# Optimization experiments

Measured on AMD Instinct MI355X. Metric: run time of the kernel, lower is better.

Reference implementation:

```python
import jax, jax.numpy as jnp
import numpy as np

S = 7; B = 2; C = 20; N = 8; BS = 16384
LAMBDA_COORD = 5.0; LAMBDA_NOOBJ = 0.5
EPS = 1e-6


def setup_inputs() -> dict:
    key = jax.random.key(0)
    k1, k2, k3 = jax.random.split(key, 3)
    outputs = jax.random.uniform(k1, (BS, S, S, B * 5 + C), dtype=jnp.float32)
    gt_boxes = jax.random.uniform(k2, (BS, N, 4), dtype=jnp.float32)
    gt_labels = jax.random.randint(k3, (BS, N), 0, C)
    return {"outputs": outputs, "gt_boxes": gt_boxes, "gt_labels": gt_labels}


def _pairwise_iou(pred_xywh, gt_boxes):
    # pred_xywh: [bs,S,S,B,4] (center x,y,w,h); gt_boxes: [bs,N,4] -> iou [bs,S,S,B,N]
    p = pred_xywh[..., None, :]                       # [bs,S,S,B,1,4]
    g = gt_boxes[:, None, None, None, :, :]           # [bs,1,1,1,N,4]
    px1, py1 = p[..., 0] - p[..., 2] / 2, p[..., 1] - p[..., 3] / 2
    px2, py2 = p[..., 0] + p[..., 2] / 2, p[..., 1] + p[..., 3] / 2
    gx1, gy1 = g[..., 0] - g[..., 2] / 2, g[..., 1] - g[..., 3] / 2
    gx2, gy2 = g[..., 0] + g[..., 2] / 2, g[..., 1] + g[..., 3] / 2
    iw = jnp.clip(jnp.minimum(px2, gx2) - jnp.maximum(px1, gx1), 0.0)
    ih = jnp.clip(jnp.minimum(py2, gy2) - jnp.maximum(py1, gy1), 0.0)
    inter = iw * ih
    union = p[..., 2] * p[..., 3] + g[..., 2] * g[..., 3] - inter
    return inter / (union + EPS)


def reference(outputs, gt_boxes, gt_labels):
    bs = outputs.shape[0]
    pred = outputs[..., : B * 5].reshape(bs, S, S, B, 5)   # [bs,S,S,B,5]
    pred_xywh, pred_conf = pred[..., :4], pred[..., 4]
    pred_cls = outputs[..., B * 5:]                        # [bs,S,S,C]

    iou = _pairwise_iou(pred_xywh, gt_boxes)               # [bs,S,S,B,N]

    # Original loop: for each gt j, if iou(:,j).max() > best -> best_iou, best_box_idx = argmax over B.
    iou_max_over_b = jnp.max(iou, axis=3)                  # [bs,S,S,N]
    j_star = jnp.argmax(iou_max_over_b, axis=-1)
    best_iou = jnp.max(iou_max_over_b, axis=-1)            # [bs,S,S]
    iou_at_j = jnp.take_along_axis(iou, j_star[..., None, None], axis=4)[..., 0]  # [bs,S,S,B]
    best_b = jnp.argmax(iou_at_j, axis=-1)                 # [bs,S,S] in [0,B)

    # Faithful to source: gt_boxes indexed by best_box_idx (the pred-box index), requires N >= B.
    gt_sel = jnp.take_along_axis(
        jnp.broadcast_to(gt_boxes[:, None, None], (bs, S, S, N, 4)),
        best_b[..., None, None], axis=3)[..., 0, :]        # [bs,S,S,4]
    pred_sel = jnp.take_along_axis(pred, best_b[..., None, None], axis=3)[..., 0, :]  # [bs,S,S,5]

    loc = ((pred_sel[..., 0] - gt_sel[..., 0]) ** 2
           + (pred_sel[..., 1] - gt_sel[..., 1]) ** 2
           + (jnp.sqrt(pred_sel[..., 2]) - jnp.sqrt(gt_sel[..., 2])) ** 2
           + (jnp.sqrt(pred_sel[..., 3]) - jnp.sqrt(gt_sel[..., 3])) ** 2)
    loc = LAMBDA_COORD * loc                               # [bs,S,S]

    conf_obj = (pred_sel[..., 4] - best_iou) ** 2          # [bs,S,S]

    # Classification: mean cross-entropy of the cell's class logits vs all gt labels
    logp = jax.nn.log_softmax(pred_cls, axis=-1)           # [bs,S,S,C]
    lab = jnp.broadcast_to(gt_labels[:, None, None, :], (bs, S, S, N))
    ce = -jnp.mean(jnp.take_along_axis(logp, lab, axis=3), axis=-1)  # [bs,S,S]

    noobj = LAMBDA_NOOBJ * jnp.sum(pred_conf ** 2, axis=-1)  # [bs,S,S]

    has_obj = best_iou > 0.0
    per_cell = jnp.where(has_obj, loc + conf_obj + ce, noobj)
    return jnp.sum(per_cell) / bs
```

## Files before the change

### kernel.cpp

```cpp
#include <hip/hip_runtime.h>

namespace {

constexpr int kS = 7;
constexpr int kC = 20;
constexpr int kN = 8;
constexpr int kBS = 16384;
constexpr int kCells = kBS * kS * kS;
constexpr int kTile = 256;
constexpr int kBlocks = kCells / kTile;
constexpr int kF = 30;
constexpr float kLambdaCoord = 5.0f;
constexpr float kLambdaNoobj = 0.5f;
constexpr float kEps = 1e-6f;

typedef const __attribute__((address_space(1))) unsigned int gu32;
typedef __attribute__((address_space(3))) unsigned int lu32;

__global__ __launch_bounds__(256) void yolo_loss_kernel(
    const float* __restrict__ outputs,
    const float* __restrict__ gt_boxes,
    const int* __restrict__ gt_labels,
    float* __restrict__ partials) {
  __shared__ float lds[kTile * kF];
  __shared__ float ws[4];

  const int tid = threadIdx.x;
  const int lane = tid & 63;
  const int w = tid >> 6;

  {
    const char* srcb = reinterpret_cast<const char*>(outputs) +
                       ((size_t)blockIdx.x * kTile + (size_t)w * 64) * 120;
    char* dstb = reinterpret_cast<char*>(lds) + w * 7680;
#pragma unroll
    for (int k = 0; k < 7; ++k) {
      __builtin_amdgcn_global_load_lds((gu32*)(srcb + k * 1024 + lane * 16),
                                       (lu32*)(dstb + k * 1024 + lane * 16),
                                       16, 0, 0);
    }
    if (lane < 32) {
      __builtin_amdgcn_global_load_lds((gu32*)(srcb + 7168 + lane * 16),
                                       (lu32*)(dstb + 7168 + lane * 16),
                                       16, 0, 0);
    }
  }

  const int c = blockIdx.x * kTile + tid;
  const int bs = c / (kS * kS);
  float g[kN][4];
  const float4* gb4 =
      reinterpret_cast<const float4*>(gt_boxes + (size_t)bs * kN * 4);
#pragma unroll
  for (int n = 0; n < kN; ++n) {
    float4 v = gb4[n];
    g[n][0] = v.x; g[n][1] = v.y; g[n][2] = v.z; g[n][3] = v.w;
  }
  const int4* lb4 = reinterpret_cast<const int4*>(gt_labels + (size_t)bs * kN);
  const int4 lab0 = lb4[0];
  const int4 lab1 = lb4[1];

  float gx1[kN], gx2[kN], gy1[kN], gy2[kN], ga[kN];
#pragma unroll
  for (int n = 0; n < kN; ++n) {
    gx1[n] = g[n][0] - g[n][2] * 0.5f;
    gx2[n] = g[n][0] + g[n][2] * 0.5f;
    gy1[n] = g[n][1] - g[n][3] * 0.5f;
    gy2[n] = g[n][1] + g[n][3] * 0.5f;
    ga[n]  = g[n][2] * g[n][3];
  }

  asm volatile("s_waitcnt vmcnt(0)" ::: "memory");

  const float* x = lds + tid * kF;

  float iou[2][kN];
#pragma unroll
  for (int b = 0; b < 2; ++b) {
    const float px = x[b * 5 + 0], py = x[b * 5 + 1];
    const float pw = x[b * 5 + 2], ph = x[b * 5 + 3];
    const float px1 = px - pw * 0.5f, px2 = px + pw * 0.5f;
    const float py1 = py - ph * 0.5f, py2 = py + ph * 0.5f;
    const float parea = pw * ph;
#pragma unroll
    for (int n = 0; n < kN; ++n) {
      const float iw = fmaxf(fminf(px2, gx2[n]) - fmaxf(px1, gx1[n]), 0.0f);
      const float ih = fmaxf(fminf(py2, gy2[n]) - fmaxf(py1, gy1[n]), 0.0f);
      const float inter = iw * ih;
      const float uni = parea + ga[n] - inter;
      iou[b][n] = inter * __builtin_amdgcn_rcpf(uni + kEps);
    }
  }

  float best_iou = -1.0f;
  float i0j = 0.0f, i1j = 0.0f;
#pragma unroll
  for (int n = 0; n < kN; ++n) {
    const float m = fmaxf(iou[0][n], iou[1][n]);
    if (m > best_iou) { best_iou = m; i0j = iou[0][n]; i1j = iou[1][n]; }
  }
  const int bb = (i1j > i0j) ? 1 : 0;

  const float gsx = bb ? g[1][0] : g[0][0];
  const float gsy = bb ? g[1][1] : g[0][1];
  const float gsw = bb ? g[1][2] : g[0][2];
  const float gsh = bb ? g[1][3] : g[0][3];
  const float psx = bb ? x[5] : x[0];
  const float psy = bb ? x[6] : x[1];
  const float psw = bb ? x[7] : x[2];
  const float psh = bb ? x[8] : x[3];
  const float psc = bb ? x[9] : x[4];

  const float dx = psx - gsx;
  const float dy = psy - gsy;
  const float dw = __builtin_amdgcn_sqrtf(psw) - __builtin_amdgcn_sqrtf(gsw);
  const float dh = __builtin_amdgcn_sqrtf(psh) - __builtin_amdgcn_sqrtf(gsh);
  const float loc = kLambdaCoord * (dx * dx + dy * dy + dw * dw + dh * dh);
  const float conf_obj = (psc - best_iou) * (psc - best_iou);

  float se = 0.0f;
#pragma unroll
  for (int k = 0; k < kC; ++k) se += __expf(x[10 + k]);
  const float lse = __logf(se);

  float ce = 0.0f;
  ce += x[10 + lab0.x] + x[10 + lab0.y] + x[10 + lab0.z] + x[10 + lab0.w];
  ce += x[10 + lab1.x] + x[10 + lab1.y] + x[10 + lab1.z] + x[10 + lab1.w];
  ce = -(ce - 8.0f * lse) * (1.0f / kN);

  const float noobj = kLambdaNoobj * (x[4] * x[4] + x[9] * x[9]);

  float val = (best_iou > 0.0f) ? (loc + conf_obj + ce) : noobj;

#pragma unroll
  for (int off = 32; off > 0; off >>= 1) val += __shfl_down(val, off, 64);
  if (lane == 0) ws[w] = val;
  __syncthreads();
  if (tid == 0) {
    partials[blockIdx.x] = ws[0] + ws[1] + ws[2] + ws[3];
  }
}

__global__ __launch_bounds__(256) void reduce_kernel(
    const float* __restrict__ partials, float* __restrict__ out) {
  float s = 0.0f;
  for (int i = threadIdx.x; i < kBlocks; i += 256) s += partials[i];
#pragma unroll
  for (int off = 32; off > 0; off >>= 1) s += __shfl_down(s, off, 64);
  __shared__ float ws[4];
  const int lane = threadIdx.x & 63;
  const int wid = threadIdx.x >> 6;
  if (lane == 0) ws[wid] = s;
  __syncthreads();
  if (threadIdx.x == 0) {
    out[0] = (ws[0] + ws[1] + ws[2] + ws[3]) * (1.0f / kBS);
  }
}

}

extern "C" void kernel_launch(void* const* d_in, const int* in_sizes, int n_in,
                              void* d_out, int out_size, void* d_ws, size_t ws_size,
                              hipStream_t stream) {
  const float* outputs = (const float*)d_in[0];
  const float* gt_boxes = (const float*)d_in[1];
  const int* gt_labels = (const int*)d_in[2];
  float* out = (float*)d_out;
  float* partials = (float*)d_ws;

  yolo_loss_kernel<<<kBlocks, kTile, 0, stream>>>(outputs, gt_boxes, gt_labels, partials);
  reduce_kernel<<<1, 256, 0, stream>>>(partials, out);
}
```

Measured before the change: 27.13 us.

## Process two tiles per block with double-buffered LDS and overlapped compute

Each block now stages two 256-cell tiles into separate LDS buffers and uses a partial vmcnt wait. Compute on the first tile can then start while the second tile's async global-to-LDS loads are still in flight. Per-sample gt values, including the sqrt of the first two box widths and heights, are packed once per tile, and the cross-entropy expression is simplified. The grid is halved, and LDS per block doubles to about 60KB, which together with higher register pressure may reduce occupancy and latency hiding.

```diff
diff --git a/kernel.cpp b/kernel.cpp
--- a/kernel.cpp
+++ b/kernel.cpp
@@ -8,7 +8,8 @@
 constexpr int kBS = 16384;
 constexpr int kCells = kBS * kS * kS;
 constexpr int kTile = 256;
-constexpr int kBlocks = kCells / kTile;
+constexpr int kTiles = kCells / kTile;
+constexpr int kBlocks = kTiles / 2;
 constexpr int kF = 30;
 constexpr float kLambdaCoord = 5.0f;
 constexpr float kLambdaNoobj = 0.5f;
@@ -17,63 +18,51 @@
 typedef const __attribute__((address_space(1))) unsigned int gu32;
 typedef __attribute__((address_space(3))) unsigned int lu32;
 
-__global__ __launch_bounds__(256) void yolo_loss_kernel(
-    const float* __restrict__ outputs,
-    const float* __restrict__ gt_boxes,
-    const int* __restrict__ gt_labels,
-    float* __restrict__ partials) {
-  __shared__ float lds[kTile * kF];
-  __shared__ float ws[4];
-
-  const int tid = threadIdx.x;
-  const int lane = tid & 63;
-  const int w = tid >> 6;
-
-  {
-    const char* srcb = reinterpret_cast<const char*>(outputs) +
-                       ((size_t)blockIdx.x * kTile + (size_t)w * 64) * 120;
-    char* dstb = reinterpret_cast<char*>(lds) + w * 7680;
-#pragma unroll
-    for (int k = 0; k < 7; ++k) {
-      __builtin_amdgcn_global_load_lds((gu32*)(srcb + k * 1024 + lane * 16),
-                                       (lu32*)(dstb + k * 1024 + lane * 16),
-                                       16, 0, 0);
-    }
-    if (lane < 32) {
-      __builtin_amdgcn_global_load_lds((gu32*)(srcb + 7168 + lane * 16),
-                                       (lu32*)(dstb + 7168 + lane * 16),
-                                       16, 0, 0);
-    }
-  }
-
-  const int c = blockIdx.x * kTile + tid;
-  const int bs = c / (kS * kS);
-  float g[kN][4];
-  const float4* gb4 =
-      reinterpret_cast<const float4*>(gt_boxes + (size_t)bs * kN * 4);
+__device__ __forceinline__ void stage_wave(const char* __restrict__ srcb,
+                                           char* dstb, int lane) {
+#pragma unroll
+  for (int k = 0; k < 7; ++k) {
+    __builtin_amdgcn_global_load_lds((gu32*)(srcb + k * 1024 + lane * 16),
+                                     (lu32*)(dstb + k * 1024 + lane * 16),
+                                     16, 0, 0);
+  }
+  if (lane < 32) {
+    __builtin_amdgcn_global_load_lds((gu32*)(srcb + 7168 + lane * 16),
+                                     (lu32*)(dstb + 7168 + lane * 16),
+                                     16, 0, 0);
+  }
+}
+
+struct GtPack {
+  float g0x, g0y, g1x, g1y;
+  float sg0w, sg0h, sg1w, sg1h;
+  float gx1[kN], gx2[kN], gy1[kN], gy2[kN], ga[kN];
+  int4 la, lb;
+};
+
+__device__ __forceinline__ GtPack make_pack(const float g[kN][4], int4 la,
+                                            int4 lb) {
+  GtPack P;
+  P.g0x = g[0][0]; P.g0y = g[0][1];
+  P.g1x = g[1][0]; P.g1y = g[1][1];
+  P.sg0w = __builtin_amdgcn_sqrtf(g[0][2]);
+  P.sg0h = __builtin_amdgcn_sqrtf(g[0][3]);
+  P.sg1w = __builtin_amdgcn_sqrtf(g[1][2]);
+  P.sg1h = __builtin_amdgcn_sqrtf(g[1][3]);
 #pragma unroll
   for (int n = 0; n < kN; ++n) {
-    float4 v = gb4[n];
-    g[n][0] = v.x; g[n][1] = v.y; g[n][2] = v.z; g[n][3] = v.w;
-  }
-  const int4* lb4 = reinterpret_cast<const int4*>(gt_labels + (size_t)bs * kN);
-  const int4 lab0 = lb4[0];
-  const int4 lab1 = lb4[1];
-
-  float gx1[kN], gx2[kN], gy1[kN], gy2[kN], ga[kN];
-#pragma unroll
-  for (int n = 0; n < kN; ++n) {
-    gx1[n] = g[n][0] - g[n][2] * 0.5f;
-    gx2[n] = g[n][0] + g[n][2] * 0.5f;
-    gy1[n] = g[n][1] - g[n][3] * 0.5f;
-    gy2[n] = g[n][1] + g[n][3] * 0.5f;
-    ga[n]  = g[n][2] * g[n][3];
-  }
-
-  asm volatile("s_waitcnt vmcnt(0)" ::: "memory");
-
-  const float* x = lds + tid * kF;
-
+    P.gx1[n] = g[n][0] - g[n][2] * 0.5f;
+    P.gx2[n] = g[n][0] + g[n][2] * 0.5f;
+    P.gy1[n] = g[n][1] - g[n][3] * 0.5f;
+    P.gy2[n] = g[n][1] + g[n][3] * 0.5f;
+    P.ga[n]  = g[n][2] * g[n][3];
+  }
+  P.la = la; P.lb = lb;
+  return P;
+}
+
+__device__ __forceinline__ float cell_loss(const float* __restrict__ x,
+                                           const GtPack& P) {
   float iou[2][kN];
 #pragma unroll
   for (int b = 0; b < 2; ++b) {
@@ -84,10 +73,10 @@
     const float parea = pw * ph;
 #pragma unroll
     for (int n = 0; n < kN; ++n) {
-      const float iw = fmaxf(fminf(px2, gx2[n]) - fmaxf(px1, gx1[n]), 0.0f);
-      const float ih = fmaxf(fminf(py2, gy2[n]) - fmaxf(py1, gy1[n]), 0.0f);
+      const float iw = fmaxf(fminf(px2, P.gx2[n]) - fmaxf(px1, P.gx1[n]), 0.0f);
+      const float ih = fmaxf(fminf(py2, P.gy2[n]) - fmaxf(py1, P.gy1[n]), 0.0f);
       const float inter = iw * ih;
-      const float uni = parea + ga[n] - inter;
+      const float uni = parea + P.ga[n] - inter;
       iou[b][n] = inter * __builtin_amdgcn_rcpf(uni + kEps);
     }
   }
@@ -101,10 +90,10 @@
   }
   const int bb = (i1j > i0j) ? 1 : 0;
 
-  const float gsx = bb ? g[1][0] : g[0][0];
-  const float gsy = bb ? g[1][1] : g[0][1];
-  const float gsw = bb ? g[1][2] : g[0][2];
-  const float gsh = bb ? g[1][3] : g[0][3];
+  const float gsx = bb ? P.g1x : P.g0x;
+  const float gsy = bb ? P.g1y : P.g0y;
+  const float sgw = bb ? P.sg1w : P.sg0w;
+  const float sgh = bb ? P.sg1h : P.sg0h;
   const float psx = bb ? x[5] : x[0];
   const float psy = bb ? x[6] : x[1];
   const float psw = bb ? x[7] : x[2];
@@ -113,8 +102,8 @@
 
   const float dx = psx - gsx;
   const float dy = psy - gsy;
-  const float dw = __builtin_amdgcn_sqrtf(psw) - __builtin_amdgcn_sqrtf(gsw);
-  const float dh = __builtin_amdgcn_sqrtf(psh) - __builtin_amdgcn_sqrtf(gsh);
+  const float dw = __builtin_amdgcn_sqrtf(psw) - sgw;
+  const float dh = __builtin_amdgcn_sqrtf(psh) - sgh;
   const float loc = kLambdaCoord * (dx * dx + dy * dy + dw * dw + dh * dh);
   const float conf_obj = (psc - best_iou) * (psc - best_iou);
 
@@ -123,14 +112,73 @@
   for (int k = 0; k < kC; ++k) se += __expf(x[10 + k]);
   const float lse = __logf(se);
 
-  float ce = 0.0f;
-  ce += x[10 + lab0.x] + x[10 + lab0.y] + x[10 + lab0.z] + x[10 + lab0.w];
-  ce += x[10 + lab1.x] + x[10 + lab1.y] + x[10 + lab1.z] + x[10 + lab1.w];
-  ce = -(ce - 8.0f * lse) * (1.0f / kN);
+  float s8 = 0.0f;
+  s8 += x[10 + P.la.x] + x[10 + P.la.y] + x[10 + P.la.z] + x[10 + P.la.w];
+  s8 += x[10 + P.lb.x] + x[10 + P.lb.y] + x[10 + P.lb.z] + x[10 + P.lb.w];
+  const float ce = lse - 0.125f * s8;
 
   const float noobj = kLambdaNoobj * (x[4] * x[4] + x[9] * x[9]);
 
-  float val = (best_iou > 0.0f) ? (loc + conf_obj + ce) : noobj;
+  return (best_iou > 0.0f) ? (loc + conf_obj + ce) : noobj;
+}
+
+__global__ __launch_bounds__(256) void yolo_loss_kernel(
+    const float* __restrict__ outputs,
+    const float* __restrict__ gt_boxes,
+    const int* __restrict__ gt_labels,
+    float* __restrict__ partials) {
+  __shared__ float lds[2][kTile * kF];
+  __shared__ float ws[4];
+
+  const int tid = threadIdx.x;
+  const int lane = tid & 63;
+  const int w = tid >> 6;
+
+  const int t0 = blockIdx.x * 2;
+  const int c0 = t0 * kTile + tid;
+  const int c1 = c0 + kTile;
+  const int bs0 = c0 / (kS * kS);
+  const int bs1 = c1 / (kS * kS);
+
+  float g0[kN][4], g1[kN][4];
+  {
+    const float4* a = reinterpret_cast<const float4*>(gt_boxes + (size_t)bs0 * kN * 4);
+    const float4* b = reinterpret_cast<const float4*>(gt_boxes + (size_t)bs1 * kN * 4);
+#pragma unroll
+    for (int n = 0; n < kN; ++n) {
+      float4 v = a[n];
+      g0[n][0] = v.x; g0[n][1] = v.y; g0[n][2] = v.z; g0[n][3] = v.w;
+    }
+#pragma unroll
+    for (int n = 0; n < kN; ++n) {
+      float4 v = b[n];
+      g1[n][0] = v.x; g1[n][1] = v.y; g1[n][2] = v.z; g1[n][3] = v.w;
+    }
+  }
+  const int4* la4 = reinterpret_cast<const int4*>(gt_labels + (size_t)bs0 * kN);
+  const int4 l0a = la4[0], l0b = la4[1];
+  const int4* lb4 = reinterpret_cast<const int4*>(gt_labels + (size_t)bs1 * kN);
+  const int4 l1a = lb4[0], l1b = lb4[1];
+
+  {
+    const char* base = reinterpret_cast<const char*>(outputs);
+    stage_wave(base + (size_t)t0 * 30720 + w * 7680,
+               reinterpret_cast<char*>(lds[0]) + w * 7680, lane);
+    stage_wave(base + (size_t)(t0 + 1) * 30720 + w * 7680,
+               reinterpret_cast<char*>(lds[1]) + w * 7680, lane);
+  }
+
+  const GtPack P0 = make_pack(g0, l0a, l0b);
+
+  asm volatile("s_waitcnt vmcnt(8)" ::: "memory");
+
+  float val = cell_loss(&lds[0][tid * kF], P0);
+
+  const GtPack P1 = make_pack(g1, l1a, l1b);
+
+  asm volatile("s_waitcnt vmcnt(0)" ::: "memory");
+
+  val += cell_loss(&lds[1][tid * kF], P1);
 
 #pragma unroll
   for (int off = 32; off > 0; off >>= 1) val += __shfl_down(val, off, 64);
```

Measured after the change: 29.22 us. 7.7% more time.
